# Performance work log

Measured on AMD Instinct MI355X. Metric: run time of the kernel, lower is better.

## Reference

```python
import jax, jax.numpy as jnp
import numpy as np

B, L, E = 8, 512, 256
H = W = 128
NH = 8
HD = E // NH


def setup_inputs() -> dict:
    key = jax.random.key(0)
    ks = jax.random.split(key, 8)
    return {
        "query_row": jax.random.normal(ks[0], (B, L, E), jnp.float32),
        "query_col": jax.random.normal(ks[1], (B, L, E), jnp.float32),
        "key_row": jax.random.normal(ks[2], (B, H, W, E), jnp.float32),
        "key_col": jax.random.normal(ks[3], (B, H, W, E), jnp.float32),
        "value": jax.random.normal(ks[4], (B, H, W, E), jnp.float32),
        "in_proj_weight": jax.random.normal(ks[5], (5 * E, E), jnp.float32) * 0.02,
        "in_proj_bias": jnp.zeros((5 * E,), jnp.float32),
        "out_proj_weight": jax.random.normal(ks[6], (E, E), jnp.float32) * 0.02,
        "out_proj_bias": jnp.zeros((E,), jnp.float32),
    }


def reference(query_row, query_col, key_row, key_col, value,
              in_proj_weight, in_proj_bias, out_proj_weight, out_proj_bias):
    b, tgt_len, embed_dim = query_row.shape
    h, w = key_col.shape[1], key_row.shape[2]
    nh, hd = NH, embed_dim // NH
    scale = float(hd) ** -0.5

    def proj(x, i):
        Wi = in_proj_weight[i * embed_dim:(i + 1) * embed_dim]
        bi = in_proj_bias[i * embed_dim:(i + 1) * embed_dim]
        return x @ Wi.T + bi

    q_row = proj(query_row, 0) * scale            # [B,L,E]
    q_col = proj(query_col, 1) * scale            # [B,L,E]
    k_row = proj(key_row, 2).mean(axis=1)         # mean over H -> [B,W,E]
    k_col = proj(key_col, 3).mean(axis=2)         # mean over W -> [B,H,E]
    v = proj(value, 4)                            # [B,H,W,E]

    def heads(x):  # [..., E] -> [B, nh, ..., hd]
        return x.reshape(x.shape[:-1] + (nh, hd))

    q_row_h = heads(q_row).transpose(0, 2, 1, 3)        # [B,nh,L,hd]
    q_col_h = heads(q_col).transpose(0, 2, 1, 3)        # [B,nh,L,hd]
    k_row_h = heads(k_row).transpose(0, 2, 1, 3)        # [B,nh,W,hd]
    k_col_h = heads(k_col).transpose(0, 2, 1, 3)        # [B,nh,H,hd]
    v_h = heads(v).transpose(0, 3, 1, 2, 4)             # [B,nh,H,W,hd]

    a_row = jax.nn.softmax(jnp.einsum('bnld,bnwd->bnlw', q_row_h, k_row_h), axis=-1)
    a_col = jax.nn.softmax(jnp.einsum('bnld,bnhd->bnlh', q_col_h, k_col_h), axis=-1)

    # contract over H first, then over W (matches torch's src_len_col >= src_len_row branch)
    ao_col = jnp.einsum('bnlh,bnhwc->bnlwc', a_col, v_h)      # [B,nh,L,W,hd]
    out = jnp.einsum('bnlw,bnlwc->bnlc', a_row, ao_col)       # [B,nh,L,hd]

    out = out.transpose(2, 0, 1, 3).reshape(tgt_len, b, embed_dim)  # [L,B,E]
    return out @ out_proj_weight.T + out_proj_bias
```

## Files before the change

### kernel.cpp

```cpp
#include <hip/hip_runtime.h>
#include <stdint.h>

#define B_  8
#define L_  512
#define E_  256
#define H_  128
#define W_  128
#define NH_ 8
#define HD_ 32

typedef unsigned short ushort_t;
typedef __attribute__((ext_vector_type(8))) short bf16x8;
typedef __attribute__((ext_vector_type(4))) float f32x4;

__device__ __forceinline__ float bf2f(ushort_t u) {
    union { unsigned int i; float f; } x;
    x.i = ((unsigned int)u) << 16;
    return x.f;
}
__device__ __forceinline__ ushort_t f2bf(float f) {
    union { float f; unsigned int i; } x;
    x.f = f;
    unsigned int r = x.i + 0x7FFFu + ((x.i >> 16) & 1u);
    return (ushort_t)(r >> 16);
}

__global__ __launch_bounds__(256) void mean_h_kernel(const float* __restrict__ kr,
                                                     float* __restrict__ out) {
    int i = blockIdx.x * 256 + threadIdx.x;
    int e = i & (E_ - 1);
    int w = (i >> 8) & (W_ - 1);
    int b = i >> 15;
    const float* p = kr + ((size_t)b * H_ * W_ + w) * E_ + e;
    float s = 0.f;
#pragma unroll 8
    for (int h = 0; h < H_; ++h) s += p[(size_t)h * W_ * E_];
    out[i] = s * (1.0f / H_);
}
__global__ __launch_bounds__(256) void mean_w_kernel(const float* __restrict__ kc,
                                                     float* __restrict__ out) {
    int i = blockIdx.x * 256 + threadIdx.x;
    int e = i & (E_ - 1);
    int h = (i >> 8) & (H_ - 1);
    int b = i >> 15;
    const float* p = kc + ((size_t)(b * H_ + h) * W_) * E_ + e;
    float s = 0.f;
#pragma unroll 8
    for (int w = 0; w < W_; ++w) s += p[(size_t)w * E_];
    out[i] = s * (1.0f / W_);
}

__device__ __forceinline__ void load4f(const float* p, float* v) {
    float4 t = *(const float4*)p;
    v[0] = t.x; v[1] = t.y; v[2] = t.z; v[3] = t.w;
}
__device__ __forceinline__ void store4(float* p, float a, float b, float c, float d) {
    float4 t; t.x = a; t.y = b; t.z = c; t.w = d;
    *(float4*)p = t;
}

__global__ __launch_bounds__(256) void gemm256(const float* __restrict__ A,
                                               const float* __restrict__ Wt,
                                               const float* __restrict__ bias,
                                               float* __restrict__ C, int M, float scale) {
    __shared__ __align__(16) float As[16][64];
    __shared__ __align__(16) float Bs[16][64];
    const int m0 = blockIdx.x * 64;
    const int n0 = blockIdx.y * 64;
    const int tid = threadIdx.x;
    const int lr = tid >> 2;
    const int lk = (tid & 3) << 2;
    const int tx = tid & 15, ty = tid >> 4;
    float acc[4][4] = {{0.f}};

    for (int k0 = 0; k0 < E_; k0 += 16) {
        float av[4], wv[4];
        load4f(A + (size_t)(m0 + lr) * E_ + k0 + lk, av);
        load4f(Wt + (size_t)(n0 + lr) * E_ + k0 + lk, wv);
        As[lk + 0][lr] = av[0]; As[lk + 1][lr] = av[1];
        As[lk + 2][lr] = av[2]; As[lk + 3][lr] = av[3];
        Bs[lk + 0][lr] = wv[0]; Bs[lk + 1][lr] = wv[1];
        Bs[lk + 2][lr] = wv[2]; Bs[lk + 3][lr] = wv[3];
        __syncthreads();
#pragma unroll
        for (int k = 0; k < 16; ++k) {
            float a[4], b[4];
            load4f(&As[k][ty << 2], a);
            load4f(&Bs[k][tx << 2], b);
#pragma unroll
            for (int i = 0; i < 4; ++i)
#pragma unroll
                for (int j = 0; j < 4; ++j) acc[i][j] += a[i] * b[j];
        }
        __syncthreads();
    }
    float bv[4];
    load4f(bias + n0 + (tx << 2), bv);
#pragma unroll
    for (int i = 0; i < 4; ++i) {
        float* cp = C + (size_t)(m0 + (ty << 2) + i) * E_ + n0 + (tx << 2);
        store4(cp, scale * (acc[i][0] + bv[0]), scale * (acc[i][1] + bv[1]),
                   scale * (acc[i][2] + bv[2]), scale * (acc[i][3] + bv[3]));
    }
}

__global__ __launch_bounds__(256) void wconv_kernel(const float* __restrict__ w,
                                                    ushort_t* __restrict__ wbf) {
    int i = (blockIdx.x * 256 + threadIdx.x) * 4;
    float4 f = *(const float4*)(w + i);
    ushort4 u;
    u.x = f2bf(f.x); u.y = f2bf(f.y); u.z = f2bf(f.z); u.w = f2bf(f.w);
    *(ushort4*)(wbf + i) = u;
}

#define KP_ 264
__global__ __launch_bounds__(256, 4) void vproj_mfma(const float* __restrict__ Ag,
                                                     const ushort_t* __restrict__ Wbf,
                                                     const float* __restrict__ bias,
                                                     ushort_t* __restrict__ v_t) {
    __shared__ ushort_t A_lds[64 * KP_];
    const int m0 = blockIdx.x * 64;
    const int tid = threadIdx.x, lane = tid & 63, wv = tid >> 6;
    const int quad = lane >> 4, lc = lane & 15;
    {
        int r = tid >> 2, c0 = (tid & 3) * 4;
        const float* sa = Ag + (size_t)(m0 + r) * 256 + c0;
        ushort_t* da = A_lds + r * KP_ + c0;
#pragma unroll
        for (int j = 0; j < 16; ++j) {
            float4 f = *(const float4*)(sa + j * 16);
            ushort4 u;
            u.x = f2bf(f.x); u.y = f2bf(f.y); u.z = f2bf(f.z); u.w = f2bf(f.w);
            *(ushort4*)(da + j * 16) = u;
        }
    }
    __syncthreads();

    f32x4 acc[4][4];
#pragma unroll
    for (int t = 0; t < 4; ++t)
#pragma unroll
        for (int et = 0; et < 4; ++et) {
            acc[t][et][0] = 0.f; acc[t][et][1] = 0.f;
            acc[t][et][2] = 0.f; acc[t][et][3] = 0.f;
        }

    const ushort_t* wrow = Wbf + (size_t)(wv * 64 + lc) * 256 + quad * 8;

    bf16x8 wf[4], wn[4];
#pragma unroll
    for (int et = 0; et < 4; ++et)
        wf[et] = *(const bf16x8*)(wrow + (size_t)(et * 16) * 256);

#pragma unroll
    for (int kc = 0; kc < 8; ++kc) {
        bf16x8 vf[4];
#pragma unroll
        for (int t = 0; t < 4; ++t)
            vf[t] = *(const bf16x8*)(A_lds + (t * 16 + lc) * KP_ + kc * 32 + quad * 8);
        if (kc < 7) {
#pragma unroll
            for (int et = 0; et < 4; ++et)
                wn[et] = *(const bf16x8*)(wrow + (size_t)(et * 16) * 256 + (kc + 1) * 32);
        }
#pragma unroll
        for (int et = 0; et < 4; ++et)
#pragma unroll
            for (int t = 0; t < 4; ++t)
                acc[t][et] = __builtin_amdgcn_mfma_f32_16x16x32_bf16(vf[t], wf[et], acc[t][et], 0, 0, 0);
#pragma unroll
        for (int et = 0; et < 4; ++et) wf[et] = wn[et];
    }

    const int b = m0 >> 14;
    const int ml = m0 & 16383;
    ushort_t* vtb = v_t + (size_t)b * 4194304 + ml + quad * 4;
#pragma unroll
    for (int et = 0; et < 4; ++et) {
        const int e = wv * 64 + et * 16 + lc;
        const float bv = bias[e];
        ushort_t* vte = vtb + (size_t)e * 16384;
#pragma unroll
        for (int t = 0; t < 4; ++t) {
            ushort4 u;
            u.x = f2bf(acc[t][et][0] + bv);
            u.y = f2bf(acc[t][et][1] + bv);
            u.z = f2bf(acc[t][et][2] + bv);
            u.w = f2bf(acc[t][et][3] + bv);
            *(ushort4*)(vte + t * 16) = u;
        }
    }
}

__global__ __launch_bounds__(256) void scores_row(const float* __restrict__ q,
                                                  const float* __restrict__ k,
                                                  float* __restrict__ a) {
    const int lt = blockIdx.x, bn = blockIdx.y;
    const int n = bn & 7, b = bn >> 3;
    const int tid = threadIdx.x;
    __shared__ float ks[128][36];
    {
        int r = tid >> 1, c16 = (tid & 1) * 16;
        const float* src = k + ((size_t)b * 128 + r) * 256 + n * 32 + c16;
#pragma unroll
        for (int j = 0; j < 4; ++j) {
            float4 f = *(const float4*)(src + j * 4);
            ks[r][c16 + j * 4 + 0] = f.x; ks[r][c16 + j * 4 + 1] = f.y;
            ks[r][c16 + j * 4 + 2] = f.z; ks[r][c16 + j * 4 + 3] = f.w;
        }
    }
    const int ll = tid >> 3, wq = tid & 7;
    float4 q4r[8];
    {
        const float* qp = q + ((size_t)b * 512 + lt * 32 + ll) * 256 + n * 32;
#pragma unroll
        for (int c4 = 0; c4 < 8; ++c4) q4r[c4] = *(const float4*)(qp + c4 * 4);
    }
    __syncthreads();
    float dots[16];
#pragma unroll
    for (int j = 0; j < 16; ++j) dots[j] = 0.f;
#pragma unroll
    for (int c4 = 0; c4 < 8; ++c4) {
        float4 q4 = q4r[c4];
#pragma unroll
        for (int j = 0; j < 16; ++j) {
            float4 k4 = *(const float4*)&ks[j * 8 + wq][c4 * 4];
            dots[j] += q4.x * k4.x + q4.y * k4.y + q4.z * k4.z + q4.w * k4.w;
        }
    }
    float mx = dots[0];
#pragma unroll
    for (int j = 1; j < 16; ++j) mx = fmaxf(mx, dots[j]);
    for (int d = 1; d < 8; d <<= 1) mx = fmaxf(mx, __shfl_xor(mx, d, 64));
    float ex[16], sm = 0.f;
#pragma unroll
    for (int j = 0; j < 16; ++j) { ex[j] = __expf(dots[j] - mx); sm += ex[j]; }
    for (int d = 1; d < 8; d <<= 1) sm += __shfl_xor(sm, d, 64);
    float inv = 1.0f / sm;
    float* ap = a + ((size_t)bn * 512 + lt * 32 + ll) * 128 + wq;
#pragma unroll
    for (int j = 0; j < 16; ++j) ap[j * 8] = ex[j] * inv;
}

__global__ __launch_bounds__(256) void scores_col(const float* __restrict__ q,
                                                  const float* __restrict__ k,
                                                  float* __restrict__ ac_t) {
    const int lt = blockIdx.x, bn = blockIdx.y;
    const int n = bn & 7, b = bn >> 3;
    const int tid = threadIdx.x;
    __shared__ float qs[32][36];
    __shared__ float sc[128][33];
    __shared__ float mxr[8][32], smr[8][32], fin[2][32];
    {
        int r = tid >> 3, c4 = (tid & 7) * 4;
        float4 f = *(const float4*)(q + ((size_t)b * 512 + lt * 32 + r) * 256 + n * 32 + c4);
        qs[r][c4 + 0] = f.x; qs[r][c4 + 1] = f.y; qs[r][c4 + 2] = f.z; qs[r][c4 + 3] = f.w;
    }
    const int h = tid >> 1, lq = tid & 1;
    float4 kk[8];
    {
        const float* kp = k + ((size_t)b * 128 + h) * 256 + n * 32;
#pragma unroll
        for (int c4 = 0; c4 < 8; ++c4) kk[c4] = *(const float4*)(kp + c4 * 4);
    }
    __syncthreads();
    float dots[16];
#pragma unroll
    for (int j = 0; j < 16; ++j) dots[j] = 0.f;
#pragma unroll
    for (int c4 = 0; c4 < 8; ++c4) {
        float4 k4 = kk[c4];
#pragma unroll
        for (int j = 0; j < 16; ++j) {
            float4 q4 = *(const float4*)&qs[j * 2 + lq][c4 * 4];
            dots[j] += k4.x * q4.x + k4.y * q4.y + k4.z * q4.z + k4.w * q4.w;
        }
    }
#pragma unroll
    for (int j = 0; j < 16; ++j) sc[h][j * 2 + lq] = dots[j];
    __syncthreads();
    {
        int lcol = tid & 31, seg = tid >> 5;
        float m = -3.0e38f;
#pragma unroll
        for (int i = 0; i < 16; ++i) m = fmaxf(m, sc[seg * 16 + i][lcol]);
        mxr[seg][lcol] = m;
    }
    __syncthreads();
    if (tid < 32) {
        float m = mxr[0][tid];
#pragma unroll
        for (int s = 1; s < 8; ++s) m = fmaxf(m, mxr[s][tid]);
        fin[0][tid] = m;
    }
    __syncthreads();
    {
        int lcol = tid & 31, seg = tid >> 5;
        float m = fin[0][lcol], s = 0.f;
#pragma unroll
        for (int i = 0; i < 16; ++i) s += __expf(sc[seg * 16 + i][lcol] - m);
        smr[seg][lcol] = s;
    }
    __syncthreads();
    if (tid < 32) {
        float t = 0.f;
#pragma unroll
        for (int s = 1; s < 8; ++s) t += smr[s][tid];
        fin[1][tid] = 1.0f / (t + smr[0][tid]);
    }
    __syncthreads();
    {
        const int lh = (tid & 1) * 16;
        float* op = ac_t + ((size_t)bn * 128 + h) * 512 + lt * 32;
#pragma unroll
        for (int j4 = 0; j4 < 4; ++j4) {
            int l0 = lh + j4 * 4;
            float4 o;
            o.x = __expf(sc[h][l0 + 0] - fin[0][l0 + 0]) * fin[1][l0 + 0];
            o.y = __expf(sc[h][l0 + 1] - fin[0][l0 + 1]) * fin[1][l0 + 1];
            o.z = __expf(sc[h][l0 + 2] - fin[0][l0 + 2]) * fin[1][l0 + 2];
            o.w = __expf(sc[h][l0 + 3] - fin[0][l0 + 3]) * fin[1][l0 + 3];
            *(float4*)(op + l0) = o;
        }
    }
}

#define ARP 136
#define VBP 136
__global__ __launch_bounds__(512, 2) void core_mfma(const float* __restrict__ a_row,
                                                    const float* __restrict__ ac_t,
                                                    const ushort_t* __restrict__ v_t,
                                                    float* __restrict__ attn) {
    __shared__ ushort_t ar_lds[128 * ARP];
    __shared__ ushort_t vb_lds[2][64 * VBP];
    const int blk = blockIdx.x;
    const int ltg = blk >> 6, bn = blk & 63;
    const int n = bn & 7, b = bn >> 3;
    const int tid = threadIdx.x, lane = tid & 63, wv = tid >> 6;
    const int quad = lane >> 4, lc = lane & 15;

    const ushort_t* vtb = v_t + (size_t)b * 4194304 + (size_t)(n * 32) * 16384;
    const int sc_ = tid >> 4, sw = (tid & 15) * 8;

    uint4 p0, p1;
    {
        const ushort_t* s0 = vtb + (size_t)sc_ * 16384 + sw;
        p0 = *(const uint4*)s0;
        p1 = *(const uint4*)(s0 + 128);
    }

    {
        const size_t abase = ((size_t)bn * L_ + ltg * 128) * 128;
        int r = tid >> 2, c0 = (tid & 3) * 4;
        const float* src = a_row + abase + (size_t)r * 128 + c0;
        ushort_t* dst = ar_lds + r * ARP + c0;
#pragma unroll
        for (int j = 0; j < 8; ++j) {
            float4 f = *(const float4*)(src + j * 16);
            ushort4 u;
            u.x = f2bf(f.x); u.y = f2bf(f.y); u.z = f2bf(f.z); u.w = f2bf(f.w);
            *(ushort4*)(dst + j * 16) = u;
        }
    }
    {
        ushort_t* d0 = vb_lds[0] + sc_ * VBP + sw;
        *(uint4*)d0 = p0;
        *(uint4*)(d0 + 32 * VBP) = p1;
    }
    __syncthreads();

    const float* act = ac_t + (size_t)bn * 65536 + ltg * 128 + wv * 16 + quad * 4;
    bf16x8 A[4];
#pragma unroll
    for (int kc = 0; kc < 4; ++kc)
        A[kc] = *(const bf16x8*)(ar_lds + (wv * 16 + lc) * ARP + kc * 32 + quad * 8);

    f32x4 acc0 = {0.f,0.f,0.f,0.f}, acc1 = {0.f,0.f,0.f,0.f};
    for (int i = 0; i < 64; ++i) {
        const int hh = i * 2, buf = i & 1;
        if (i < 63) {
            const ushort_t* s0 = vtb + (size_t)sc_ * 16384 + (hh + 2) * 128 + sw;
            p0 = *(const uint4*)s0;
            p1 = *(const uint4*)(s0 + 128);
        }
        float4 av0 = *(const float4*)(act + (size_t)hh * 512);
        float4 av1 = *(const float4*)(act + (size_t)(hh + 1) * 512);
        const ushort_t* vb0 = vb_lds[buf];
        const ushort_t* vb1 = vb_lds[buf] + 32 * VBP;
        f32x4 t0 = {0.f,0.f,0.f,0.f}, t1 = {0.f,0.f,0.f,0.f};
        f32x4 u0 = {0.f,0.f,0.f,0.f}, u1 = {0.f,0.f,0.f,0.f};
#pragma unroll
        for (int kc = 0; kc < 4; ++kc) {
            const int ko = kc * 32 + quad * 8;
            bf16x8 b0 = *(const bf16x8*)(vb0 + lc * VBP + ko);
            bf16x8 b1 = *(const bf16x8*)(vb0 + (16 + lc) * VBP + ko);
            bf16x8 c0 = *(const bf16x8*)(vb1 + lc * VBP + ko);
            bf16x8 c1 = *(const bf16x8*)(vb1 + (16 + lc) * VBP + ko);
            t0 = __builtin_amdgcn_mfma_f32_16x16x32_bf16(A[kc], b0, t0, 0, 0, 0);
            t1 = __builtin_amdgcn_mfma_f32_16x16x32_bf16(A[kc], b1, t1, 0, 0, 0);
            u0 = __builtin_amdgcn_mfma_f32_16x16x32_bf16(A[kc], c0, u0, 0, 0, 0);
            u1 = __builtin_amdgcn_mfma_f32_16x16x32_bf16(A[kc], c1, u1, 0, 0, 0);
        }
        acc0[0] += av0.x * t0[0] + av1.x * u0[0]; acc1[0] += av0.x * t1[0] + av1.x * u1[0];
        acc0[1] += av0.y * t0[1] + av1.y * u0[1]; acc1[1] += av0.y * t1[1] + av1.y * u1[1];
        acc0[2] += av0.z * t0[2] + av1.z * u0[2]; acc1[2] += av0.z * t1[2] + av1.z * u1[2];
        acc0[3] += av0.w * t0[3] + av1.w * u0[3]; acc1[3] += av0.w * t1[3] + av1.w * u1[3];
        if (i < 63) {
            ushort_t* d0 = vb_lds[buf ^ 1] + sc_ * VBP + sw;
            *(uint4*)d0 = p0;
            *(uint4*)(d0 + 32 * VBP) = p1;
            __syncthreads();
        }
    }
    const int row0 = wv * 16 + quad * 4;
#pragma unroll
    for (int r = 0; r < 4; ++r) {
        size_t o = ((size_t)(ltg * 128 + row0 + r) * B_ + b) * E_ + n * HD_ + lc;
        attn[o] = acc0[r];
        attn[o + 16] = acc1[r];
    }
}

extern "C" void kernel_launch(void* const* d_in, const int* in_sizes, int n_in,
                              void* d_out, int out_size, void* d_ws, size_t ws_size,
                              hipStream_t stream) {
    const float* query_row = (const float*)d_in[0];
    const float* query_col = (const float*)d_in[1];
    const float* key_row   = (const float*)d_in[2];
    const float* key_col   = (const float*)d_in[3];
    const float* value     = (const float*)d_in[4];
    const float* ipw       = (const float*)d_in[5];
    const float* ipb       = (const float*)d_in[6];
    const float* opw       = (const float*)d_in[7];
    const float* opb       = (const float*)d_in[8];
    float* out = (float*)d_out;

    char* ws = (char*)d_ws;
    float* q_row_s = (float*)ws;  ws += (size_t)4096 * 256 * 4;
    float* q_col_s = (float*)ws;  ws += (size_t)4096 * 256 * 4;
    float* krm     = (float*)ws;  ws += (size_t)262144 * 4;
    float* kcm     = (float*)ws;  ws += (size_t)262144 * 4;
    float* k_row   = (float*)ws;  ws += (size_t)262144 * 4;
    float* k_col   = (float*)ws;  ws += (size_t)262144 * 4;
    ushort_t* v_t  = (ushort_t*)ws; ws += (size_t)33554432 * 2;
    float* a_row   = (float*)ws;  ws += (size_t)4194304 * 4;
    float* ac_t    = (float*)ws;  ws += (size_t)4194304 * 4;
    float* attn    = (float*)ws;  ws += (size_t)4096 * 256 * 4;
    ushort_t* wbf  = (ushort_t*)ws; ws += (size_t)65536 * 2;

    const float scale = 0.17677669529663687f;

    mean_h_kernel<<<1024, 256, 0, stream>>>(key_row, krm);
    mean_w_kernel<<<1024, 256, 0, stream>>>(key_col, kcm);
    wconv_kernel<<<64, 256, 0, stream>>>(ipw + 4 * 65536, wbf);

    gemm256<<<dim3(64, 4), 256, 0, stream>>>(query_row, ipw + 0 * 65536, ipb + 0,    q_row_s, 4096, scale);
    gemm256<<<dim3(64, 4), 256, 0, stream>>>(query_col, ipw + 1 * 65536, ipb + 256,  q_col_s, 4096, scale);
    gemm256<<<dim3(16, 4), 256, 0, stream>>>(krm,       ipw + 2 * 65536, ipb + 512,  k_row,   1024, 1.0f);
    gemm256<<<dim3(16, 4), 256, 0, stream>>>(kcm,       ipw + 3 * 65536, ipb + 768,  k_col,   1024, 1.0f);

    vproj_mfma<<<2048, 256, 0, stream>>>(value, wbf, ipb + 1024, v_t);

    scores_row<<<dim3(16, 64), 256, 0, stream>>>(q_row_s, k_row, a_row);
    scores_col<<<dim3(16, 64), 256, 0, stream>>>(q_col_s, k_col, ac_t);

    core_mfma<<<256, 512, 0, stream>>>(a_row, ac_t, v_t, attn);

    gemm256<<<dim3(64, 4), 256, 0, stream>>>(attn, opw, opb, out, 4096, 1.0f);
}
```

Measured before the change: 589.1 us.

## Vectorize mean kernels, drop LDS staging in vproj, store row attention as bf16

The mean-over-H and mean-over-W kernels now read and write float4 per thread, and launch a quarter as many blocks. vproj_mfma drops its LDS staging and reads fp32 value rows straight from global memory, converting them with the hardware packed bf16 convert instruction, which also replaces the software rounding on its output. scores_row writes the row softmax as bf16, so core_mfma reads half the bytes and skips its own conversion. Together these aim to cut memory traffic and conversion ALU work. The cost is that vproj loses its weight-prefetch double buffering and now issues uncoalesced strided global loads for the A operand.

Measured after the change: 629.6 us. 1.07x slower.

```diff
diff --git a/kernel.cpp b/kernel.cpp
--- a/kernel.cpp
+++ b/kernel.cpp
@@ -24,30 +24,43 @@
     unsigned int r = x.i + 0x7FFFu + ((x.i >> 16) & 1u);
     return (ushort_t)(r >> 16);
 }
+__device__ __forceinline__ unsigned int cvt_pk_bf16(float lo, float hi) {
+    unsigned int r;
+    asm("v_cvt_pk_bf16_f32 %0, %1, %2" : "=v"(r) : "v"(lo), "v"(hi));
+    return r;
+}
 
 __global__ __launch_bounds__(256) void mean_h_kernel(const float* __restrict__ kr,
                                                      float* __restrict__ out) {
     int i = blockIdx.x * 256 + threadIdx.x;
-    int e = i & (E_ - 1);
-    int w = (i >> 8) & (W_ - 1);
-    int b = i >> 15;
-    const float* p = kr + ((size_t)b * H_ * W_ + w) * E_ + e;
-    float s = 0.f;
-#pragma unroll 8
-    for (int h = 0; h < H_; ++h) s += p[(size_t)h * W_ * E_];
-    out[i] = s * (1.0f / H_);
+    int e4 = i & 63, w = (i >> 6) & 127, b = i >> 13;
+    const float* p = kr + ((size_t)b * 16384 + w) * 256 + e4 * 4;
+    float4 s = {0.f, 0.f, 0.f, 0.f};
+#pragma unroll 4
+    for (int h = 0; h < H_; ++h) {
+        float4 f = *(const float4*)(p + (size_t)h * 32768);
+        s.x += f.x; s.y += f.y; s.z += f.z; s.w += f.w;
+    }
+    float4 o;
+    o.x = s.x * (1.0f / H_); o.y = s.y * (1.0f / H_);
+    o.z = s.z * (1.0f / H_); o.w = s.w * (1.0f / H_);
+    *(float4*)(out + (size_t)i * 4) = o;
 }
 __global__ __launch_bounds__(256) void mean_w_kernel(const float* __restrict__ kc,
                                                      float* __restrict__ out) {
     int i = blockIdx.x * 256 + threadIdx.x;
-    int e = i & (E_ - 1);
-    int h = (i >> 8) & (H_ - 1);
-    int b = i >> 15;
-    const float* p = kc + ((size_t)(b * H_ + h) * W_) * E_ + e;
-    float s = 0.f;
-#pragma unroll 8
-    for (int w = 0; w < W_; ++w) s += p[(size_t)w * E_];
-    out[i] = s * (1.0f / W_);
+    int e4 = i & 63, h = (i >> 6) & 127, b = i >> 13;
+    const float* p = kc + ((size_t)(b * 128 + h) * 128) * 256 + e4 * 4;
+    float4 s = {0.f, 0.f, 0.f, 0.f};
+#pragma unroll 4
+    for (int w = 0; w < W_; ++w) {
+        float4 f = *(const float4*)(p + (size_t)w * 256);
+        s.x += f.x; s.y += f.y; s.z += f.z; s.w += f.w;
+    }
+    float4 o;
+    o.x = s.x * (1.0f / W_); o.y = s.y * (1.0f / W_);
+    o.z = s.z * (1.0f / W_); o.w = s.w * (1.0f / W_);
+    *(float4*)(out + (size_t)i * 4) = o;
 }
 
 __device__ __forceinline__ void load4f(const float* p, float* v) {
@@ -113,28 +126,16 @@
     *(ushort4*)(wbf + i) = u;
 }
 
-#define KP_ 264
 __global__ __launch_bounds__(256, 4) void vproj_mfma(const float* __restrict__ Ag,
                                                      const ushort_t* __restrict__ Wbf,
                                                      const float* __restrict__ bias,
                                                      ushort_t* __restrict__ v_t) {
-    __shared__ ushort_t A_lds[64 * KP_];
     const int m0 = blockIdx.x * 64;
     const int tid = threadIdx.x, lane = tid & 63, wv = tid >> 6;
     const int quad = lane >> 4, lc = lane & 15;
-    {
-        int r = tid >> 2, c0 = (tid & 3) * 4;
-        const float* sa = Ag + (size_t)(m0 + r) * 256 + c0;
-        ushort_t* da = A_lds + r * KP_ + c0;
-#pragma unroll
-        for (int j = 0; j < 16; ++j) {
-            float4 f = *(const float4*)(sa + j * 16);
-            ushort4 u;
-            u.x = f2bf(f.x); u.y = f2bf(f.y); u.z = f2bf(f.z); u.w = f2bf(f.w);
-            *(ushort4*)(da + j * 16) = u;
-        }
-    }
-    __syncthreads();
+
+    const float* vrow = Ag + ((size_t)(m0 + lc)) * 256 + quad * 8;
+    const ushort_t* wrow = Wbf + (size_t)(wv * 64 + lc) * 256 + quad * 8;
 
     f32x4 acc[4][4];
 #pragma unroll
@@ -145,31 +146,30 @@
             acc[t][et][2] = 0.f; acc[t][et][3] = 0.f;
         }
 
-    const ushort_t* wrow = Wbf + (size_t)(wv * 64 + lc) * 256 + quad * 8;
-
-    bf16x8 wf[4], wn[4];
-#pragma unroll
-    for (int et = 0; et < 4; ++et)
-        wf[et] = *(const bf16x8*)(wrow + (size_t)(et * 16) * 256);
-
 #pragma unroll
     for (int kc = 0; kc < 8; ++kc) {
         bf16x8 vf[4];
 #pragma unroll
-        for (int t = 0; t < 4; ++t)
-            vf[t] = *(const bf16x8*)(A_lds + (t * 16 + lc) * KP_ + kc * 32 + quad * 8);
-        if (kc < 7) {
-#pragma unroll
-            for (int et = 0; et < 4; ++et)
-                wn[et] = *(const bf16x8*)(wrow + (size_t)(et * 16) * 256 + (kc + 1) * 32);
-        }
+        for (int t = 0; t < 4; ++t) {
+            const float* vp = vrow + (size_t)(t * 16) * 256 + kc * 32;
+            float4 f0 = *(const float4*)vp;
+            float4 f1 = *(const float4*)(vp + 4);
+            union { bf16x8 v; unsigned int u[4]; } pk;
+            pk.u[0] = cvt_pk_bf16(f0.x, f0.y);
+            pk.u[1] = cvt_pk_bf16(f0.z, f0.w);
+            pk.u[2] = cvt_pk_bf16(f1.x, f1.y);
+            pk.u[3] = cvt_pk_bf16(f1.z, f1.w);
+            vf[t] = pk.v;
+        }
+        bf16x8 wf[4];
+#pragma unroll
+        for (int et = 0; et < 4; ++et)
+            wf[et] = *(const bf16x8*)(wrow + (size_t)(et * 16) * 256 + kc * 32);
 #pragma unroll
         for (int et = 0; et < 4; ++et)
 #pragma unroll
             for (int t = 0; t < 4; ++t)
                 acc[t][et] = __builtin_amdgcn_mfma_f32_16x16x32_bf16(vf[t], wf[et], acc[t][et], 0, 0, 0);
-#pragma unroll
-        for (int et = 0; et < 4; ++et) wf[et] = wn[et];
     }
 
     const int b = m0 >> 14;
@@ -182,19 +182,17 @@
         ushort_t* vte = vtb + (size_t)e * 16384;
 #pragma unroll
         for (int t = 0; t < 4; ++t) {
-            ushort4 u;
-            u.x = f2bf(acc[t][et][0] + bv);
-            u.y = f2bf(acc[t][et][1] + bv);
-            u.z = f2bf(acc[t][et][2] + bv);
-            u.w = f2bf(acc[t][et][3] + bv);
-            *(ushort4*)(vte + t * 16) = u;
+            union { ushort4 u4; unsigned int w[2]; } uu;
+            uu.w[0] = cvt_pk_bf16(acc[t][et][0] + bv, acc[t][et][1] + bv);
+            uu.w[1] = cvt_pk_bf16(acc[t][et][2] + bv, acc[t][et][3] + bv);
+            *(ushort4*)(vte + t * 16) = uu.u4;
         }
     }
 }
 
 __global__ __launch_bounds__(256) void scores_row(const float* __restrict__ q,
                                                   const float* __restrict__ k,
-                                                  float* __restrict__ a) {
+                                                  ushort_t* __restrict__ a) {
     const int lt = blockIdx.x, bn = blockIdx.y;
     const int n = bn & 7, b = bn >> 3;
     const int tid = threadIdx.x;
@@ -238,9 +236,9 @@
     for (int j = 0; j < 16; ++j) { ex[j] = __expf(dots[j] - mx); sm += ex[j]; }
     for (int d = 1; d < 8; d <<= 1) sm += __shfl_xor(sm, d, 64);
     float inv = 1.0f / sm;
-    float* ap = a + ((size_t)bn * 512 + lt * 32 + ll) * 128 + wq;
-#pragma unroll
-    for (int j = 0; j < 16; ++j) ap[j * 8] = ex[j] * inv;
+    ushort_t* ap = a + ((size_t)bn * 512 + lt * 32 + ll) * 128 + wq;
+#pragma unroll
+    for (int j = 0; j < 16; ++j) ap[j * 8] = f2bf(ex[j] * inv);
 }
 
 __global__ __launch_bounds__(256) void scores_col(const float* __restrict__ q,
@@ -328,7 +326,7 @@
 
 #define ARP 136
 #define VBP 136
-__global__ __launch_bounds__(512, 2) void core_mfma(const float* __restrict__ a_row,
+__global__ __launch_bounds__(512, 2) void core_mfma(const ushort_t* __restrict__ a_row,
                                                     const float* __restrict__ ac_t,
                                                     const ushort_t* __restrict__ v_t,
                                                     float* __restrict__ attn) {
@@ -353,15 +351,11 @@
     {
         const size_t abase = ((size_t)bn * L_ + ltg * 128) * 128;
         int r = tid >> 2, c0 = (tid & 3) * 4;
-        const float* src = a_row + abase + (size_t)r * 128 + c0;
+        const ushort_t* src = a_row + abase + (size_t)r * 128 + c0;
         ushort_t* dst = ar_lds + r * ARP + c0;
 #pragma unroll
-        for (int j = 0; j < 8; ++j) {
-            float4 f = *(const float4*)(src + j * 16);
-            ushort4 u;
-            u.x = f2bf(f.x); u.y = f2bf(f.y); u.z = f2bf(f.z); u.w = f2bf(f.w);
-            *(ushort4*)(dst + j * 16) = u;
-        }
+        for (int j = 0; j < 8; ++j)
+            *(ushort4*)(dst + j * 16) = *(const ushort4*)(src + j * 16);
     }
     {
         ushort_t* d0 = vb_lds[0] + sc_ * VBP + sw;
@@ -444,15 +438,15 @@
     float* k_row   = (float*)ws;  ws += (size_t)262144 * 4;
     float* k_col   = (float*)ws;  ws += (size_t)262144 * 4;
     ushort_t* v_t  = (ushort_t*)ws; ws += (size_t)33554432 * 2;
-    float* a_row   = (float*)ws;  ws += (size_t)4194304 * 4;
+    ushort_t* a_row = (ushort_t*)ws; ws += (size_t)4194304 * 2;
     float* ac_t    = (float*)ws;  ws += (size_t)4194304 * 4;
     float* attn    = (float*)ws;  ws += (size_t)4096 * 256 * 4;
     ushort_t* wbf  = (ushort_t*)ws; ws += (size_t)65536 * 2;
 
     const float scale = 0.17677669529663687f;
 
-    mean_h_kernel<<<1024, 256, 0, stream>>>(key_row, krm);
-    mean_w_kernel<<<1024, 256, 0, stream>>>(key_col, kcm);
+    mean_h_kernel<<<256, 256, 0, stream>>>(key_row, krm);
+    mean_w_kernel<<<256, 256, 0, stream>>>(key_col, kcm);
     wconv_kernel<<<64, 256, 0, stream>>>(ipw + 4 * 65536, wbf);
 
     gemm256<<<dim3(64, 4), 256, 0, stream>>>(query_row, ipw + 0 * 65536, ipb + 0,    q_row_s, 4096, scale);
```
